# Optimization experiments

Hardware: AMD Instinct MI355X
Metric: run time of the kernel (lower is better)

The kernel has to match this reference:

```python
import jax, jax.numpy as jnp
from jax import lax
import numpy as np

GROUPS = 32  # EMA 'factor'
EPS = 1e-5   # torch GroupNorm default eps


def setup_inputs() -> dict:
    key = jax.random.key(0)
    ks = jax.random.split(key, 3)
    B, C, H, W = 8, 256, 128, 128
    cg = C // GROUPS  # channels per group = 8
    x = jax.random.normal(ks[0], (B, C, H, W), dtype=jnp.float32)
    w1 = jax.random.normal(ks[1], (cg, cg), dtype=jnp.float32) * 0.1    # conv1x1 weight (O,I)
    b1 = jnp.zeros((cg,), dtype=jnp.float32)
    w3 = jax.random.normal(ks[2], (cg, cg, 3, 3), dtype=jnp.float32) * 0.1  # conv3x3 weight (O,I,kh,kw)
    b3 = jnp.zeros((cg,), dtype=jnp.float32)
    gn_w = jnp.ones((cg,), dtype=jnp.float32)
    gn_b = jnp.zeros((cg,), dtype=jnp.float32)
    return {"x": x, "w1": w1, "b1": b1, "w3": w3, "b3": b3, "gn_w": gn_w, "gn_b": gn_b}


def reference(x, w1, b1, w3, b3, gn_w, gn_b):
    b, c, h, w = x.shape
    g = GROUPS
    cg = c // g
    gx = x.reshape(b * g, cg, h, w)                       # [bg, cg, h, w]
    # directional pooling (AdaptiveAvgPool over one axis)
    x_h = gx.mean(axis=3, keepdims=True)                  # [bg, cg, h, 1]
    x_w = gx.mean(axis=2, keepdims=True).transpose(0, 1, 3, 2)  # [bg, cg, w, 1]
    hw = jnp.concatenate([x_h, x_w], axis=2)              # [bg, cg, h+w, 1]
    hw = jnp.einsum('oi,bilk->bolk', w1, hw) + b1[None, :, None, None]
    xh = hw[:, :, :h]                                      # [bg, cg, h, 1]
    xw = hw[:, :, h:].transpose(0, 1, 3, 2)                # [bg, cg, 1, w]
    gated = gx * jax.nn.sigmoid(xh) * jax.nn.sigmoid(xw)
    # GroupNorm(cg groups over cg channels) == per-channel norm over (h, w)
    mu = gated.mean(axis=(2, 3), keepdims=True)
    var = gated.var(axis=(2, 3), keepdims=True)
    x1 = (gated - mu) / jnp.sqrt(var + EPS) * gn_w[None, :, None, None] + gn_b[None, :, None, None]
    # 3x3 conv branch
    x2 = lax.conv_general_dilated(gx, w3, (1, 1), 'SAME',
                                  dimension_numbers=('NCHW', 'OIHW', 'NCHW'))
    x2 = x2 + b3[None, :, None, None]
    # cross-branch channel-attention matmuls
    x11 = jax.nn.softmax(x1.mean(axis=(2, 3)), axis=-1)[:, None, :]  # [bg, 1, cg]
    x21 = jax.nn.softmax(x2.mean(axis=(2, 3)), axis=-1)[:, None, :]  # [bg, 1, cg]
    x12 = x2.reshape(b * g, cg, h * w)
    x22 = x1.reshape(b * g, cg, h * w)
    weights = (jnp.matmul(x11, x12) + jnp.matmul(x21, x22)).reshape(b * g, 1, h, w)
    return (gx * jax.nn.sigmoid(weights)).reshape(b, c, h, w)
```

## Files before the change

kernel.cpp:

```cpp
#include <hip/hip_runtime.h>
#include <cstdint>

#define EPS 1e-5f

#define LDS_TL    0
#define LDS_SH    35904
#define LDS_SW    36928
#define LDS_S     37952
#define LDS_TM    37960
#define LDS_CORN  38032
#define LDS_M2    38064
#define LDS_X11   38072
#define LDS_X21   38080
#define LDS_W1L   38088
#define LDS_B1L   38152
#define LDS_WTL   38160
#define LDS_PS    38240
#define LDS_QS    38304
#define LDS_AL    38368
#define LDS_BS    38376
#define LDS_BETA  38384
#define LDS_TOTAL 38400

__global__ __launch_bounds__(1024) void fused_adaptatt(
    const float* __restrict__ x,
    const float* __restrict__ w1, const float* __restrict__ b1,
    const float* __restrict__ w3, const float* __restrict__ b3,
    const float* __restrict__ gn_w, const float* __restrict__ gn_b,
    float* __restrict__ out)
{
    extern __shared__ float lds[];
    const int bg = blockIdx.x;
    const int t  = threadIdx.x;
    const int sg = t >> 8;
    const int ts = t & 255;
    float* rs = lds;
    float* cs = lds + 1024;
    float4* red = (float4*)(lds + 2048);
    const size_t pbase = (size_t)(bg * 8) * 16384;

    for (int half = 0; half < 2; ++half) {
        int pi = half * 4 + sg;
        const float4* xp = (const float4*)(x + pbase + (size_t)pi * 16384);
        float4 csum = {0.f, 0.f, 0.f, 0.f};
        for (int i = 0; i < 16; ++i) {
            float4 v = xp[i * 256 + ts];
            csum.x += v.x; csum.y += v.y; csum.z += v.z; csum.w += v.w;
            float rsv = v.x + v.y + v.z + v.w;
            for (int m = 16; m; m >>= 1) rsv += __shfl_xor(rsv, m);
            if ((ts & 31) == 0) rs[pi * 128 + i * 8 + (ts >> 5)] = rsv;
        }
        red[sg * 256 + ts] = csum;
        __syncthreads();
        if (ts < 32) {
            float4 s = red[sg * 256 + ts];
            for (int j = 1; j < 8; ++j) {
                float4 v = red[sg * 256 + j * 32 + ts];
                s.x += v.x; s.y += v.y; s.z += v.z; s.w += v.w;
            }
            ((float4*)(cs + pi * 128))[ts] = s;
        }
        __syncthreads();
    }

    if (t < 64) lds[LDS_W1L + t] = w1[t];
    if (t >= 64 && t < 72) lds[LDS_B1L + (t - 64)] = b1[t - 64];
    if (t >= 128 && t < 136) {
        int i = t - 128;
        const float* xpp = x + pbase + (size_t)i * 16384;
        lds[LDS_CORN + i * 4 + 0] = xpp[0];
        lds[LDS_CORN + i * 4 + 1] = xpp[127];
        lds[LDS_CORN + i * 4 + 2] = xpp[127 * 128];
        lds[LDS_CORN + i * 4 + 3] = xpp[127 * 128 + 127];
    }
    if (t == 200) {
        float mx = gn_b[0];
        for (int i = 1; i < 8; ++i) mx = fmaxf(mx, gn_b[i]);
        float e[8], s = 0.f;
        for (int i = 0; i < 8; ++i) { e[i] = __expf(gn_b[i] - mx); s += e[i]; }
        for (int i = 0; i < 8; ++i) lds[LDS_X11 + i] = e[i] / s;
    }
    __syncthreads();

    {
        int o = t >> 7, y = t & 127;
        const float inv128 = 1.f / 128.f;
        float ar = lds[LDS_B1L + o], ac = ar;
        for (int i = 0; i < 8; ++i) {
            float w = lds[LDS_W1L + o * 8 + i];
            ar += w * rs[i * 128 + y] * inv128;
            ac += w * cs[i * 128 + y] * inv128;
        }
        lds[LDS_SH + o * 128 + y] = 1.f / (1.f + __expf(-ar));
        lds[LDS_SW + o * 128 + y] = 1.f / (1.f + __expf(-ac));
    }
    if (t < 8) {
        float s = 0.f;
        for (int y = 0; y < 128; ++y) s += rs[t * 128 + y];
        lds[LDS_S + t] = s;
    }
    __syncthreads();

    if (t < 72) {
        int i = t / 9, ky = (t % 9) / 3, kx = t % 3;
        float v = lds[LDS_S + i];
        if (ky == 0) v -= rs[i * 128 + 127]; else if (ky == 2) v -= rs[i * 128 + 0];
        if (kx == 0) v -= cs[i * 128 + 127]; else if (kx == 2) v -= cs[i * 128 + 0];
        if (ky == 0 && kx == 0) v += lds[LDS_CORN + i * 4 + 3];
        if (ky == 0 && kx == 2) v += lds[LDS_CORN + i * 4 + 2];
        if (ky == 2 && kx == 0) v += lds[LDS_CORN + i * 4 + 1];
        if (ky == 2 && kx == 2) v += lds[LDS_CORN + i * 4 + 0];
        lds[LDS_TM + t] = v;
    }
    __syncthreads();

    if (t < 8) {
        float acc = 0.f;
        for (int j = 0; j < 72; ++j) acc += w3[t * 72 + j] * lds[LDS_TM + j];
        lds[LDS_M2 + t] = b3[t] + acc * (1.f / 16384.f);
    }
    if (t >= 128 && t < 201) {
        int j = t - 128;
        float a = 0.f;
        if (j < 72) { for (int o = 0; o < 8; ++o) a += lds[LDS_X11 + o] * w3[o * 72 + j]; }
        else        { for (int o = 0; o < 8; ++o) a += lds[LDS_X11 + o] * b3[o]; }
        lds[LDS_WTL + j] = a;
    }
    __syncthreads();

    if (t == 0) {
        float mx = lds[LDS_M2];
        for (int i = 1; i < 8; ++i) mx = fmaxf(mx, lds[LDS_M2 + i]);
        float e[8], s = 0.f;
        for (int i = 0; i < 8; ++i) { e[i] = __expf(lds[LDS_M2 + i] - mx); s += e[i]; }
        for (int i = 0; i < 8; ++i) lds[LDS_X21 + i] = e[i] / s;
    }
    __syncthreads();

    float* shl = lds + LDS_SH;
    float* swl = lds + LDS_SW;
    for (int half = 0; half < 2; ++half) {
        int pi = half * 4 + sg;
        const float4* xp = (const float4*)(x + pbase + (size_t)pi * 16384);
        float4 sw4 = ((const float4*)(swl + pi * 128))[ts & 31];
        float s = 0.f, q = 0.f;
        for (int i = 0; i < 16; ++i) {
            float4 v = xp[i * 256 + ts];
            float shv = shl[pi * 128 + i * 8 + (ts >> 5)];
            float g0 = v.x * shv * sw4.x;
            float g1 = v.y * shv * sw4.y;
            float g2 = v.z * shv * sw4.z;
            float g3 = v.w * shv * sw4.w;
            s += g0 + g1 + g2 + g3;
            q += g0 * g0 + g1 * g1 + g2 * g2 + g3 * g3;
        }
        for (int m = 16; m; m >>= 1) { s += __shfl_xor(s, m); q += __shfl_xor(q, m); }
        if ((ts & 31) == 0) {
            lds[LDS_PS + pi * 8 + (ts >> 5)] = s;
            lds[LDS_QS + pi * 8 + (ts >> 5)] = q;
        }
    }
    __syncthreads();
    if (t < 8) {
        float s = 0.f, q = 0.f;
        for (int j = 0; j < 8; ++j) { s += lds[LDS_PS + t * 8 + j]; q += lds[LDS_QS + t * 8 + j]; }
        float mu  = s * (1.f / 16384.f);
        float ex2 = q * (1.f / 16384.f);
        float var = ex2 - mu * mu;
        float inv = rsqrtf(var + EPS);
        float x21v = lds[LDS_X21 + t];
        lds[LDS_AL + t] = x21v * inv * gn_w[t];
        lds[LDS_BS + t] = x21v * (gn_b[t] - mu * inv * gn_w[t]);
    }
    __syncthreads();
    if (t == 0) {
        float s = lds[LDS_WTL + 72];
        for (int i = 0; i < 8; ++i) s += lds[LDS_BS + i];
        lds[LDS_BETA] = s;
    }
    __syncthreads();

    const float beta_v = lds[LDS_BETA];
    for (int ch = 0; ch < 4; ++ch) {
        int r0 = ch * 32;
        __syncthreads();
        {
            int rr = t >> 5, c4 = t & 31;
            int g = r0 - 1 + rr;
#pragma unroll
            for (int i = 0; i < 8; ++i) {
                float4 v = {0.f, 0.f, 0.f, 0.f};
                if (g >= 0 && g < 128)
                    v = *(const float4*)(x + pbase + (size_t)i * 16384 + g * 128 + c4 * 4);
                float* d = &lds[(i * 34 + rr) * 132 + 1 + c4 * 4];
                d[0] = v.x; d[1] = v.y; d[2] = v.z; d[3] = v.w;
                if (c4 == 0)  d[-1] = 0.f;
                if (c4 == 31) d[4]  = 0.f;
                if (t < 64) {
                    int rr2 = 32 + rr;
                    int g2 = r0 - 1 + rr2;
                    float4 v2 = {0.f, 0.f, 0.f, 0.f};
                    if (g2 < 128)
                        v2 = *(const float4*)(x + pbase + (size_t)i * 16384 + g2 * 128 + c4 * 4);
                    float* d2 = &lds[(i * 34 + rr2) * 132 + 1 + c4 * 4];
                    d2[0] = v2.x; d2[1] = v2.y; d2[2] = v2.z; d2[3] = v2.w;
                    if (c4 == 0)  d2[-1] = 0.f;
                    if (c4 == 31) d2[4]  = 0.f;
                }
            }
        }
        __syncthreads();
        int y = t >> 5;
        int x0 = (t & 31) * 4;
        float acc0, acc1, acc2, acc3;
        acc0 = acc1 = acc2 = acc3 = beta_v;
        float gv[8][4];
#pragma unroll
        for (int i = 0; i < 8; ++i) {
            const float* base = &lds[(i * 34 + y) * 132 + x0];
#pragma unroll
            for (int ky = 0; ky < 3; ++ky) {
                float4 va = *(const float4*)(base + ky * 132);
                float4 vb = *(const float4*)(base + ky * 132 + 4);
                float w0 = lds[LDS_WTL + i * 9 + ky * 3 + 0];
                float w1v = lds[LDS_WTL + i * 9 + ky * 3 + 1];
                float w2 = lds[LDS_WTL + i * 9 + ky * 3 + 2];
                acc0 += w0 * va.x + w1v * va.y + w2 * va.z;
                acc1 += w0 * va.y + w1v * va.z + w2 * va.w;
                acc2 += w0 * va.z + w1v * va.w + w2 * vb.x;
                acc3 += w0 * va.w + w1v * vb.x + w2 * vb.y;
                if (ky == 1) { gv[i][0] = va.y; gv[i][1] = va.z; gv[i][2] = va.w; gv[i][3] = vb.x; }
            }
            float as = lds[LDS_AL + i] * shl[i * 128 + r0 + y];
            float4 s4 = *(const float4*)(swl + i * 128 + x0);
            acc0 += as * s4.x * gv[i][0];
            acc1 += as * s4.y * gv[i][1];
            acc2 += as * s4.z * gv[i][2];
            acc3 += as * s4.w * gv[i][3];
        }
        float sg0 = 1.f / (1.f + __expf(-acc0));
        float sg1 = 1.f / (1.f + __expf(-acc1));
        float sg2 = 1.f / (1.f + __expf(-acc2));
        float sg3 = 1.f / (1.f + __expf(-acc3));
        size_t ob = pbase + (size_t)(r0 + y) * 128 + x0;
#pragma unroll
        for (int c = 0; c < 8; ++c) {
            float4 o4 = { gv[c][0] * sg0, gv[c][1] * sg1, gv[c][2] * sg2, gv[c][3] * sg3 };
            *(float4*)(out + ob + (size_t)c * 16384) = o4;
        }
    }
}

extern "C" void kernel_launch(void* const* d_in, const int* in_sizes, int n_in,
                              void* d_out, int out_size, void* d_ws, size_t ws_size,
                              hipStream_t stream) {
    (void)in_sizes; (void)n_in; (void)out_size; (void)d_ws; (void)ws_size;
    const float* x    = (const float*)d_in[0];
    const float* w1   = (const float*)d_in[1];
    const float* b1   = (const float*)d_in[2];
    const float* w3   = (const float*)d_in[3];
    const float* b3   = (const float*)d_in[4];
    const float* gn_w = (const float*)d_in[5];
    const float* gn_b = (const float*)d_in[6];
    float* out = (float*)d_out;

    hipLaunchKernelGGL(fused_adaptatt, dim3(256), dim3(1024), LDS_TOTAL * 4, stream,
                       x, w1, b1, w3, b3, gn_w, gn_b, out);
}
```

Measured before the change: 118.5 us.

## Split fused kernel into gate, stats and output kernels with finer output grid

```diff
diff --git a/kernel.cpp b/kernel.cpp
--- a/kernel.cpp
+++ b/kernel.cpp
@@ -2,41 +2,22 @@
 #include <cstdint>
 
 #define EPS 1e-5f
-
-#define LDS_TL    0
-#define LDS_SH    35904
-#define LDS_SW    36928
-#define LDS_S     37952
-#define LDS_TM    37960
-#define LDS_CORN  38032
-#define LDS_M2    38064
-#define LDS_X11   38072
-#define LDS_X21   38080
-#define LDS_W1L   38088
-#define LDS_B1L   38152
-#define LDS_WTL   38160
-#define LDS_PS    38240
-#define LDS_QS    38304
-#define LDS_AL    38368
-#define LDS_BS    38376
-#define LDS_BETA  38384
-#define LDS_TOTAL 38400
-
-__global__ __launch_bounds__(1024) void fused_adaptatt(
+#define TS 136
+
+__global__ __launch_bounds__(1024) void k1_gates(
     const float* __restrict__ x,
     const float* __restrict__ w1, const float* __restrict__ b1,
     const float* __restrict__ w3, const float* __restrict__ b3,
-    const float* __restrict__ gn_w, const float* __restrict__ gn_b,
-    float* __restrict__ out)
+    const float* __restrict__ gn_b,
+    float* __restrict__ sh, float* __restrict__ sw,
+    float* __restrict__ x21, float* __restrict__ wt)
 {
-    extern __shared__ float lds[];
+    __shared__ float rs[1024], cs[1024];
+    __shared__ float4 red[1024];
+    __shared__ float w1l[64], b1l[8], corn[32], S[8], Tm[72], m2[8], x11[8];
     const int bg = blockIdx.x;
     const int t  = threadIdx.x;
-    const int sg = t >> 8;
-    const int ts = t & 255;
-    float* rs = lds;
-    float* cs = lds + 1024;
-    float4* red = (float4*)(lds + 2048);
+    const int sg = t >> 8, ts = t & 255;
     const size_t pbase = (size_t)(bg * 8) * 16384;
 
     for (int half = 0; half < 2; ++half) {
@@ -63,82 +44,96 @@
         __syncthreads();
     }
 
-    if (t < 64) lds[LDS_W1L + t] = w1[t];
-    if (t >= 64 && t < 72) lds[LDS_B1L + (t - 64)] = b1[t - 64];
+    if (t < 64) w1l[t] = w1[t];
+    if (t >= 64 && t < 72) b1l[t - 64] = b1[t - 64];
     if (t >= 128 && t < 136) {
         int i = t - 128;
         const float* xpp = x + pbase + (size_t)i * 16384;
-        lds[LDS_CORN + i * 4 + 0] = xpp[0];
-        lds[LDS_CORN + i * 4 + 1] = xpp[127];
-        lds[LDS_CORN + i * 4 + 2] = xpp[127 * 128];
-        lds[LDS_CORN + i * 4 + 3] = xpp[127 * 128 + 127];
+        corn[i * 4 + 0] = xpp[0];
+        corn[i * 4 + 1] = xpp[127];
+        corn[i * 4 + 2] = xpp[127 * 128];
+        corn[i * 4 + 3] = xpp[127 * 128 + 127];
     }
     if (t == 200) {
         float mx = gn_b[0];
         for (int i = 1; i < 8; ++i) mx = fmaxf(mx, gn_b[i]);
         float e[8], s = 0.f;
         for (int i = 0; i < 8; ++i) { e[i] = __expf(gn_b[i] - mx); s += e[i]; }
-        for (int i = 0; i < 8; ++i) lds[LDS_X11 + i] = e[i] / s;
+        for (int i = 0; i < 8; ++i) x11[i] = e[i] / s;
     }
     __syncthreads();
 
     {
         int o = t >> 7, y = t & 127;
         const float inv128 = 1.f / 128.f;
-        float ar = lds[LDS_B1L + o], ac = ar;
+        float ar = b1l[o], ac = ar;
         for (int i = 0; i < 8; ++i) {
-            float w = lds[LDS_W1L + o * 8 + i];
+            float w = w1l[o * 8 + i];
             ar += w * rs[i * 128 + y] * inv128;
             ac += w * cs[i * 128 + y] * inv128;
         }
-        lds[LDS_SH + o * 128 + y] = 1.f / (1.f + __expf(-ar));
-        lds[LDS_SW + o * 128 + y] = 1.f / (1.f + __expf(-ac));
+        sh[(bg * 8 + o) * 128 + y] = 1.f / (1.f + __expf(-ar));
+        sw[(bg * 8 + o) * 128 + y] = 1.f / (1.f + __expf(-ac));
     }
     if (t < 8) {
         float s = 0.f;
         for (int y = 0; y < 128; ++y) s += rs[t * 128 + y];
-        lds[LDS_S + t] = s;
+        S[t] = s;
     }
     __syncthreads();
 
     if (t < 72) {
         int i = t / 9, ky = (t % 9) / 3, kx = t % 3;
-        float v = lds[LDS_S + i];
+        float v = S[i];
         if (ky == 0) v -= rs[i * 128 + 127]; else if (ky == 2) v -= rs[i * 128 + 0];
         if (kx == 0) v -= cs[i * 128 + 127]; else if (kx == 2) v -= cs[i * 128 + 0];
-        if (ky == 0 && kx == 0) v += lds[LDS_CORN + i * 4 + 3];
-        if (ky == 0 && kx == 2) v += lds[LDS_CORN + i * 4 + 2];
-        if (ky == 2 && kx == 0) v += lds[LDS_CORN + i * 4 + 1];
-        if (ky == 2 && kx == 2) v += lds[LDS_CORN + i * 4 + 0];
-        lds[LDS_TM + t] = v;
+        if (ky == 0 && kx == 0) v += corn[i * 4 + 3];
+        if (ky == 0 && kx == 2) v += corn[i * 4 + 2];
+        if (ky == 2 && kx == 0) v += corn[i * 4 + 1];
+        if (ky == 2 && kx == 2) v += corn[i * 4 + 0];
+        Tm[t] = v;
     }
     __syncthreads();
 
     if (t < 8) {
         float acc = 0.f;
-        for (int j = 0; j < 72; ++j) acc += w3[t * 72 + j] * lds[LDS_TM + j];
-        lds[LDS_M2 + t] = b3[t] + acc * (1.f / 16384.f);
-    }
-    if (t >= 128 && t < 201) {
+        for (int j = 0; j < 72; ++j) acc += w3[t * 72 + j] * Tm[j];
+        m2[t] = b3[t] + acc * (1.f / 16384.f);
+    }
+    if (bg == 0 && t >= 128 && t < 201) {
         int j = t - 128;
         float a = 0.f;
-        if (j < 72) { for (int o = 0; o < 8; ++o) a += lds[LDS_X11 + o] * w3[o * 72 + j]; }
-        else        { for (int o = 0; o < 8; ++o) a += lds[LDS_X11 + o] * b3[o]; }
-        lds[LDS_WTL + j] = a;
+        if (j < 72) { for (int o = 0; o < 8; ++o) a += x11[o] * w3[o * 72 + j]; }
+        else        { for (int o = 0; o < 8; ++o) a += x11[o] * b3[o]; }
+        wt[j] = a;
     }
     __syncthreads();
 
     if (t == 0) {
-        float mx = lds[LDS_M2];
-        for (int i = 1; i < 8; ++i) mx = fmaxf(mx, lds[LDS_M2 + i]);
+        float mx = m2[0];
+        for (int i = 1; i < 8; ++i) mx = fmaxf(mx, m2[i]);
         float e[8], s = 0.f;
-        for (int i = 0; i < 8; ++i) { e[i] = __expf(lds[LDS_M2 + i] - mx); s += e[i]; }
-        for (int i = 0; i < 8; ++i) lds[LDS_X21 + i] = e[i] / s;
-    }
-    __syncthreads();
-
-    float* shl = lds + LDS_SH;
-    float* swl = lds + LDS_SW;
+        for (int i = 0; i < 8; ++i) { e[i] = __expf(m2[i] - mx); s += e[i]; }
+        for (int i = 0; i < 8; ++i) x21[bg * 8 + i] = e[i] / s;
+    }
+}
+
+__global__ __launch_bounds__(1024) void k2_stats(
+    const float* __restrict__ x, const float* __restrict__ sh,
+    const float* __restrict__ sw, const float* __restrict__ x21,
+    const float* __restrict__ gn_w, const float* __restrict__ gn_b,
+    const float* __restrict__ wt,
+    float* __restrict__ alpha, float* __restrict__ beta)
+{
+    __shared__ float shl[1024], swl[1024], ps[64], qs[64], bs[8];
+    const int bg = blockIdx.x;
+    const int t  = threadIdx.x;
+    const int sg = t >> 8, ts = t & 255;
+    const size_t pbase = (size_t)(bg * 8) * 16384;
+    shl[t] = sh[bg * 1024 + t];
+    swl[t] = sw[bg * 1024 + t];
+    __syncthreads();
+
     for (int half = 0; half < 2; ++half) {
         int pi = half * 4 + sg;
         const float4* xp = (const float4*)(x + pbase + (size_t)pi * 16384);
@@ -156,105 +151,145 @@
         }
         for (int m = 16; m; m >>= 1) { s += __shfl_xor(s, m); q += __shfl_xor(q, m); }
         if ((ts & 31) == 0) {
-            lds[LDS_PS + pi * 8 + (ts >> 5)] = s;
-            lds[LDS_QS + pi * 8 + (ts >> 5)] = q;
+            ps[pi * 8 + (ts >> 5)] = s;
+            qs[pi * 8 + (ts >> 5)] = q;
         }
     }
     __syncthreads();
     if (t < 8) {
         float s = 0.f, q = 0.f;
-        for (int j = 0; j < 8; ++j) { s += lds[LDS_PS + t * 8 + j]; q += lds[LDS_QS + t * 8 + j]; }
+        for (int j = 0; j < 8; ++j) { s += ps[t * 8 + j]; q += qs[t * 8 + j]; }
         float mu  = s * (1.f / 16384.f);
         float ex2 = q * (1.f / 16384.f);
         float var = ex2 - mu * mu;
         float inv = rsqrtf(var + EPS);
-        float x21v = lds[LDS_X21 + t];
-        lds[LDS_AL + t] = x21v * inv * gn_w[t];
-        lds[LDS_BS + t] = x21v * (gn_b[t] - mu * inv * gn_w[t]);
+        float x21v = x21[bg * 8 + t];
+        alpha[bg * 8 + t] = x21v * inv * gn_w[t];
+        bs[t] = x21v * (gn_b[t] - mu * inv * gn_w[t]);
     }
     __syncthreads();
     if (t == 0) {
-        float s = lds[LDS_WTL + 72];
-        for (int i = 0; i < 8; ++i) s += lds[LDS_BS + i];
-        lds[LDS_BETA] = s;
-    }
-    __syncthreads();
-
-    const float beta_v = lds[LDS_BETA];
-    for (int ch = 0; ch < 4; ++ch) {
-        int r0 = ch * 32;
-        __syncthreads();
-        {
-            int rr = t >> 5, c4 = t & 31;
-            int g = r0 - 1 + rr;
-#pragma unroll
-            for (int i = 0; i < 8; ++i) {
-                float4 v = {0.f, 0.f, 0.f, 0.f};
-                if (g >= 0 && g < 128)
-                    v = *(const float4*)(x + pbase + (size_t)i * 16384 + g * 128 + c4 * 4);
-                float* d = &lds[(i * 34 + rr) * 132 + 1 + c4 * 4];
-                d[0] = v.x; d[1] = v.y; d[2] = v.z; d[3] = v.w;
-                if (c4 == 0)  d[-1] = 0.f;
-                if (c4 == 31) d[4]  = 0.f;
-                if (t < 64) {
-                    int rr2 = 32 + rr;
-                    int g2 = r0 - 1 + rr2;
-                    float4 v2 = {0.f, 0.f, 0.f, 0.f};
-                    if (g2 < 128)
-                        v2 = *(const float4*)(x + pbase + (size_t)i * 16384 + g2 * 128 + c4 * 4);
-                    float* d2 = &lds[(i * 34 + rr2) * 132 + 1 + c4 * 4];
-                    d2[0] = v2.x; d2[1] = v2.y; d2[2] = v2.z; d2[3] = v2.w;
-                    if (c4 == 0)  d2[-1] = 0.f;
-                    if (c4 == 31) d2[4]  = 0.f;
-                }
+        float s = wt[72];
+        for (int i = 0; i < 8; ++i) s += bs[i];
+        beta[bg] = s;
+    }
+}
+
+__global__ __launch_bounds__(256, 2) void k3_out(
+    const float* __restrict__ x, const float* __restrict__ sh,
+    const float* __restrict__ sw, const float* __restrict__ alpha,
+    const float* __restrict__ beta, const float* __restrict__ wt,
+    float* __restrict__ out)
+{
+    __shared__ float tl[8 * 18 * TS];
+    __shared__ float wtl[73], al[8];
+    __shared__ float betal;
+    const int blk = blockIdx.x;
+    const int bg  = blk >> 3;
+    const int r0  = (blk & 7) * 16;
+    const int t    = threadIdx.x;
+    const int lane = t & 31;
+    const int cidx = t >> 5;
+    const size_t pbase = (size_t)(bg * 8) * 16384;
+
+    {
+        const float* xc = x + pbase + (size_t)cidx * 16384 + 4 * lane;
+        float* dst = tl + (cidx * 18) * TS + 4 + 4 * lane;
+#pragma unroll
+        for (int row = 0; row < 18; ++row) {
+            int g = r0 - 1 + row;
+            float4 v = {0.f, 0.f, 0.f, 0.f};
+            if ((unsigned)g < 128u) v = *(const float4*)(xc + (size_t)g * 128);
+            *(float4*)(dst + row * TS) = v;
+        }
+        if (lane == 0 || lane == 31) {
+            float* pz = tl + (cidx * 18) * TS + (lane == 0 ? 0 : 132);
+            float4 z = {0.f, 0.f, 0.f, 0.f};
+#pragma unroll
+            for (int row = 0; row < 18; ++row) *(float4*)(pz + row * TS) = z;
+        }
+    }
+    if (t < 73) wtl[t] = wt[t];
+    else if (t < 81) al[t - 73] = alpha[bg * 8 + (t - 73)];
+    else if (t == 81) betal = beta[bg];
+    __syncthreads();
+
+    const int yg = cidx;
+    const int y0 = r0 + 2 * yg;
+    const int x0 = 4 * lane;
+    float4 accA = {betal, betal, betal, betal};
+    float4 accB = accA;
+    float4 gvA[8], gvB[8];
+
+#pragma unroll
+    for (int i = 0; i < 8; ++i) {
+        const float* B = tl + (i * 18 + 2 * yg) * TS + 4 + x0;
+        float asA = al[i] * sh[(size_t)(bg * 8 + i) * 128 + y0];
+        float asB = al[i] * sh[(size_t)(bg * 8 + i) * 128 + y0 + 1];
+        float4 s4 = *(const float4*)(sw + (size_t)(bg * 8 + i) * 128 + x0);
+#pragma unroll
+        for (int r = 0; r < 4; ++r) {
+            float4 v = *(const float4*)(B + r * TS);
+            float xm1 = __shfl_up(v.w, 1, 32);
+            if (lane == 0)  xm1 = 0.f;
+            float xp4 = __shfl_down(v.x, 1, 32);
+            if (lane == 31) xp4 = 0.f;
+            if (r < 3) {
+                float w0 = wtl[i * 9 + r * 3 + 0];
+                float w1v = wtl[i * 9 + r * 3 + 1];
+                float w2 = wtl[i * 9 + r * 3 + 2];
+                accA.x += w0 * xm1  + w1v * v.x + w2 * v.y;
+                accA.y += w0 * v.x  + w1v * v.y + w2 * v.z;
+                accA.z += w0 * v.y  + w1v * v.z + w2 * v.w;
+                accA.w += w0 * v.z  + w1v * v.w + w2 * xp4;
             }
-        }
-        __syncthreads();
-        int y = t >> 5;
-        int x0 = (t & 31) * 4;
-        float acc0, acc1, acc2, acc3;
-        acc0 = acc1 = acc2 = acc3 = beta_v;
-        float gv[8][4];
-#pragma unroll
-        for (int i = 0; i < 8; ++i) {
-            const float* base = &lds[(i * 34 + y) * 132 + x0];
-#pragma unroll
-            for (int ky = 0; ky < 3; ++ky) {
-                float4 va = *(const float4*)(base + ky * 132);
-                float4 vb = *(const float4*)(base + ky * 132 + 4);
-                float w0 = lds[LDS_WTL + i * 9 + ky * 3 + 0];
-                float w1v = lds[LDS_WTL + i * 9 + ky * 3 + 1];
-                float w2 = lds[LDS_WTL + i * 9 + ky * 3 + 2];
-                acc0 += w0 * va.x + w1v * va.y + w2 * va.z;
-                acc1 += w0 * va.y + w1v * va.z + w2 * va.w;
-                acc2 += w0 * va.z + w1v * va.w + w2 * vb.x;
-                acc3 += w0 * va.w + w1v * vb.x + w2 * vb.y;
-                if (ky == 1) { gv[i][0] = va.y; gv[i][1] = va.z; gv[i][2] = va.w; gv[i][3] = vb.x; }
+            if (r > 0) {
+                int ky = r - 1;
+                float w0 = wtl[i * 9 + ky * 3 + 0];
+                float w1v = wtl[i * 9 + ky * 3 + 1];
+                float w2 = wtl[i * 9 + ky * 3 + 2];
+                accB.x += w0 * xm1  + w1v * v.x + w2 * v.y;
+                accB.y += w0 * v.x  + w1v * v.y + w2 * v.z;
+                accB.z += w0 * v.y  + w1v * v.z + w2 * v.w;
+                accB.w += w0 * v.z  + w1v * v.w + w2 * xp4;
             }
-            float as = lds[LDS_AL + i] * shl[i * 128 + r0 + y];
-            float4 s4 = *(const float4*)(swl + i * 128 + x0);
-            acc0 += as * s4.x * gv[i][0];
-            acc1 += as * s4.y * gv[i][1];
-            acc2 += as * s4.z * gv[i][2];
-            acc3 += as * s4.w * gv[i][3];
-        }
-        float sg0 = 1.f / (1.f + __expf(-acc0));
-        float sg1 = 1.f / (1.f + __expf(-acc1));
-        float sg2 = 1.f / (1.f + __expf(-acc2));
-        float sg3 = 1.f / (1.f + __expf(-acc3));
-        size_t ob = pbase + (size_t)(r0 + y) * 128 + x0;
-#pragma unroll
-        for (int c = 0; c < 8; ++c) {
-            float4 o4 = { gv[c][0] * sg0, gv[c][1] * sg1, gv[c][2] * sg2, gv[c][3] * sg3 };
-            *(float4*)(out + ob + (size_t)c * 16384) = o4;
-        }
+            if (r == 1) gvA[i] = v;
+            if (r == 2) gvB[i] = v;
+        }
+        accA.x += asA * s4.x * gvA[i].x;
+        accA.y += asA * s4.y * gvA[i].y;
+        accA.z += asA * s4.z * gvA[i].z;
+        accA.w += asA * s4.w * gvA[i].w;
+        accB.x += asB * s4.x * gvB[i].x;
+        accB.y += asB * s4.y * gvB[i].y;
+        accB.z += asB * s4.z * gvB[i].z;
+        accB.w += asB * s4.w * gvB[i].w;
+    }
+
+    float4 sgA, sgB;
+    sgA.x = 1.f / (1.f + __expf(-accA.x));
+    sgA.y = 1.f / (1.f + __expf(-accA.y));
+    sgA.z = 1.f / (1.f + __expf(-accA.z));
+    sgA.w = 1.f / (1.f + __expf(-accA.w));
+    sgB.x = 1.f / (1.f + __expf(-accB.x));
+    sgB.y = 1.f / (1.f + __expf(-accB.y));
+    sgB.z = 1.f / (1.f + __expf(-accB.z));
+    sgB.w = 1.f / (1.f + __expf(-accB.w));
+
+    size_t ob = pbase + (size_t)y0 * 128 + x0;
+#pragma unroll
+    for (int c = 0; c < 8; ++c) {
+        float4 oA = { gvA[c].x * sgA.x, gvA[c].y * sgA.y, gvA[c].z * sgA.z, gvA[c].w * sgA.w };
+        float4 oB = { gvB[c].x * sgB.x, gvB[c].y * sgB.y, gvB[c].z * sgB.z, gvB[c].w * sgB.w };
+        *(float4*)(out + ob + (size_t)c * 16384)       = oA;
+        *(float4*)(out + ob + (size_t)c * 16384 + 128) = oB;
     }
 }
 
 extern "C" void kernel_launch(void* const* d_in, const int* in_sizes, int n_in,
                               void* d_out, int out_size, void* d_ws, size_t ws_size,
                               hipStream_t stream) {
-    (void)in_sizes; (void)n_in; (void)out_size; (void)d_ws; (void)ws_size;
+    (void)in_sizes; (void)n_in; (void)out_size; (void)ws_size;
     const float* x    = (const float*)d_in[0];
     const float* w1   = (const float*)d_in[1];
     const float* b1   = (const float*)d_in[2];
@@ -263,7 +298,19 @@
     const float* gn_w = (const float*)d_in[5];
     const float* gn_b = (const float*)d_in[6];
     float* out = (float*)d_out;
-
-    hipLaunchKernelGGL(fused_adaptatt, dim3(256), dim3(1024), LDS_TOTAL * 4, stream,
-                       x, w1, b1, w3, b3, gn_w, gn_b, out);
+    float* ws  = (float*)d_ws;
+
+    float* sh    = ws;
+    float* sw    = ws + 262144;
+    float* x21   = ws + 524288;
+    float* alpha = ws + 526336;
+    float* beta  = ws + 528384;
+    float* wt    = ws + 528640;
+
+    hipLaunchKernelGGL(k1_gates, dim3(256),  dim3(1024), 0, stream,
+                       x, w1, b1, w3, b3, gn_b, sh, sw, x21, wt);
+    hipLaunchKernelGGL(k2_stats, dim3(256),  dim3(1024), 0, stream,
+                       x, sh, sw, x21, gn_w, gn_b, wt, alpha, beta);
+    hipLaunchKernelGGL(k3_out,   dim3(2048), dim3(256),  0, stream,
+                       x, sh, sw, alpha, beta, wt, out);
 }
```

New measurement: 107.6 us. -9.3%, faster.
